# Kernel tuning notes

Hardware: AMD Instinct MI355X
Metric: run time of the kernel (lower is better)

Reference implementation:

```python
import jax, jax.numpy as jnp
import numpy as np

B, L, H, W, C = 2, 32, 16, 16, 32  # L must equal channels for the view() to be consistent
CH = L  # conv channel count


def setup_inputs() -> dict:
    key = jax.random.key(0)
    k1, k2, k3, k4, k5 = jax.random.split(key, 5)
    return {
        "inputs": jax.random.normal(k1, (B, L, H, W, C), dtype=jnp.float32),
        "W1": jax.random.normal(k2, (CH // 2, CH), dtype=jnp.float32) * 0.1,
        "b1": jax.random.normal(k3, (CH // 2,), dtype=jnp.float32) * 0.1,
        "W2": jax.random.normal(k4, (CH, CH), dtype=jnp.float32) * 0.1,
        "b2": jax.random.normal(k5, (CH,), dtype=jnp.float32) * 0.1,
        "gamma": jnp.ones((1,), dtype=jnp.float32),
    }


def reference(inputs, W1, b1, W2, b2, gamma):
    b, l, h, w, c = inputs.shape
    n = l * h * w  # flattened 'spatial' positions after the (buggy-but-faithful) reshape
    # conv1x1 over dim-1 (torch Conv3d treats dim-1 as channels)
    x1 = jnp.einsum('ol,blhwc->bohwc', W1, inputs) + b1[None, :, None, None, None]
    # permute (0,4,1,2,3) then view(b, c//2, l*h*w)
    x1 = jnp.transpose(x1, (0, 4, 1, 2, 3)).reshape(b, c // 2, n)
    # attn[b, i, j] = sum_k x1[b, k, i] * x1[b, k, j]; softmax over last dim
    attn = jax.nn.softmax(jnp.einsum('bki,bkj->bij', x1, x1), axis=-1)  # [b, n, n]
    x2 = jnp.einsum('ol,blhwc->bohwc', W2, inputs) + b2[None, :, None, None, None]
    x2 = jnp.transpose(x2, (0, 4, 1, 2, 3)).reshape(b, c, n)
    # x2 @ attn^T : out[b, c, i] = sum_j x2[b, c, j] * attn[b, i, j]
    out = jnp.einsum('bcj,bij->bci', x2, attn)
    out = jnp.transpose(out.reshape(b, c, l, h, w), (0, 2, 3, 4, 1))
    return out * gamma + inputs
```

## Files before the change

kernel.cpp:

```cpp
#include <hip/hip_runtime.h>
#include <hip/hip_bf16.h>
#include <math.h>

typedef __bf16 bf16x8 __attribute__((ext_vector_type(8)));
typedef __bf16 bf16x2 __attribute__((ext_vector_type(2)));
typedef short  s16x2  __attribute__((ext_vector_type(2)));
typedef short  s16x4  __attribute__((ext_vector_type(4)));
typedef float  floatx16 __attribute__((ext_vector_type(16)));

#define KQ_ELEMS (2 * 8192 * 16)
#define OACC_OFF 1572864
#define SQRT_LOG2E 1.2011224087864498f
#define LSPLIT 4

__global__ __launch_bounds__(256) void proj_kernel(
    const float* __restrict__ in, const float* __restrict__ W1,
    const float* __restrict__ b1, const float* __restrict__ W2,
    const float* __restrict__ b2,
    __hip_bfloat16* __restrict__ Kq, __hip_bfloat16* __restrict__ Vswz,
    float* __restrict__ acc0)
{
    __shared__ float Xs[32][32];
    __shared__ float W1s[16 * 32];
    __shared__ float W2s[32 * 32];
    const int t = threadIdx.x;
    const int bid = blockIdx.x;
    const int b = bid >> 8;
    const int hw = bid & 255;

    {
        int gid = bid * 256 + t;
        *(float4*)(acc0 + (size_t)gid * 4) = make_float4(0.f, 0.f, 0.f, 0.f);
        if (gid < 4096)
            *(float4*)(acc0 + 524288 + (size_t)gid * 4) = make_float4(0.f, 0.f, 0.f, 0.f);
    }

    {
        int l = t >> 3, cs = (t & 7) * 4;
        float4 v = *(const float4*)(in + (((size_t)b * 32 + l) * 256 + hw) * 32 + cs);
        *(float4*)&Xs[l][cs] = v;
    }
    if (t < 128) *(float4*)&W1s[t * 4] = *(const float4*)(W1 + t * 4);
    *(float4*)&W2s[t * 4] = *(const float4*)(W2 + t * 4);
    __syncthreads();

    const int c = t & 31;
    const int g = t >> 5;

#pragma unroll
    for (int oo = 0; oo < 2; ++oo) {
        int o = g * 2 + oo;
        float acc = b1[o];
#pragma unroll
        for (int l = 0; l < 32; ++l) acc += W1s[o * 32 + l] * Xs[l][c];
        int k = c >> 1;
        int i = (c & 1) * 4096 + o * 256 + hw;
        Kq[((size_t)b * 8192 + i) * 16 + k] = __float2bfloat16(acc * SQRT_LOG2E);
    }
#pragma unroll
    for (int oo = 0; oo < 4; ++oo) {
        int o = g * 4 + oo;
        float acc = b2[o];
#pragma unroll
        for (int l = 0; l < 32; ++l) acc += W2s[o * 32 + l] * Xs[l][c];
        int j = o * 256 + hw;
        int jt = j >> 5, rem = j & 31;
        int gg = rem >> 3, h = (rem >> 2) & 1, idx = rem & 3;
        Vswz[(size_t)b * 262144 + jt * 1024 + gg * 256 + h * 128 + c * 4 + idx] =
            __float2bfloat16(acc);
    }
}

__global__ __launch_bounds__(256) void flash_kernel(
    const __hip_bfloat16* __restrict__ Kq, const __hip_bfloat16* __restrict__ Vswz,
    float* __restrict__ Oacc, float* __restrict__ Lacc)
{
    const int t = threadIdx.x;
    const int lane = t & 63;
    const int wv = t >> 6;
    const int m = lane & 31;
    const int h = lane >> 5;

    const int bid = blockIdx.x;
    const int s = bid & ((1 << LSPLIT) - 1);
    const int itile = (bid >> LSPLIT) & 63;
    const int b = bid >> (LSPLIT + 6);
    const int i0 = itile * 128 + wv * 32;
    const int niter = (8192 >> LSPLIT) >> 5;
    const int jt0 = s * niter;

    const __hip_bfloat16* Kb = Kq + (size_t)b * 8192 * 16;
    const __hip_bfloat16* Vb = Vswz + (size_t)b * 262144 + h * 128 + m * 4;

    const bf16x8 bq = *(const bf16x8*)(Kb + (size_t)(i0 + m) * 16 + h * 8);

    floatx16 oa = {}, ob = {};
    float2 l01 = {0.f, 0.f}, l23 = {0.f, 0.f};

    bf16x8 ak = *(const bf16x8*)(Kb + (size_t)(jt0 * 32 + m) * 16 + h * 8);
    s16x4 vf0 = *(const s16x4*)(Vb + (size_t)jt0 * 1024 + 0);
    s16x4 vf1 = *(const s16x4*)(Vb + (size_t)jt0 * 1024 + 256);
    s16x4 vf2 = *(const s16x4*)(Vb + (size_t)jt0 * 1024 + 512);
    s16x4 vf3 = *(const s16x4*)(Vb + (size_t)jt0 * 1024 + 768);

    for (int it = 0; it < niter; ++it) {
        const int jtn = jt0 + (it + 1 < niter ? it + 1 : it);
        bf16x8 ak_n = *(const bf16x8*)(Kb + (size_t)(jtn * 32 + m) * 16 + h * 8);
        s16x4 vn0 = *(const s16x4*)(Vb + (size_t)jtn * 1024 + 0);
        s16x4 vn1 = *(const s16x4*)(Vb + (size_t)jtn * 1024 + 256);
        s16x4 vn2 = *(const s16x4*)(Vb + (size_t)jtn * 1024 + 512);
        s16x4 vn3 = *(const s16x4*)(Vb + (size_t)jtn * 1024 + 768);

        floatx16 sc = __builtin_amdgcn_mfma_f32_32x32x16_bf16(ak, bq, (floatx16){}, 0, 0, 0);

#pragma unroll
        for (int g = 0; g < 4; ++g) {
            float e0 = __builtin_amdgcn_exp2f(sc[4 * g + 0]);
            float e1 = __builtin_amdgcn_exp2f(sc[4 * g + 1]);
            float e2 = __builtin_amdgcn_exp2f(sc[4 * g + 2]);
            float e3 = __builtin_amdgcn_exp2f(sc[4 * g + 3]);
            l01.x += e0; l01.y += e1; l23.x += e2; l23.y += e3;
#if defined(__has_builtin) && __has_builtin(__builtin_amdgcn_cvt_pk_bf16_f32)
            bf16x2 plo = __builtin_amdgcn_cvt_pk_bf16_f32(e0, e1);
            bf16x2 phi = __builtin_amdgcn_cvt_pk_bf16_f32(e2, e3);
#else
            bf16x2 plo = {(__bf16)e0, (__bf16)e1};
            bf16x2 phi = {(__bf16)e2, (__bf16)e3};
#endif
            s16x2 lo = __builtin_bit_cast(s16x2, plo);
            s16x2 hi = __builtin_bit_cast(s16x2, phi);
            s16x4 pb = {lo[0], lo[1], hi[0], hi[1]};
            s16x4 vf = (g == 0) ? vf0 : (g == 1) ? vf1 : (g == 2) ? vf2 : vf3;
            if (g < 2)
                oa = __builtin_amdgcn_mfma_f32_32x32x8bf16_1k(pb, vf, oa, 0, 0, 0);
            else
                ob = __builtin_amdgcn_mfma_f32_32x32x8bf16_1k(pb, vf, ob, 0, 0, 0);
        }
        ak = ak_n; vf0 = vn0; vf1 = vn1; vf2 = vn2; vf3 = vn3;
    }

    oa = oa + ob;
    float l = (l01.x + l01.y) + (l23.x + l23.y);
    l += __shfl_xor(l, 32);

#pragma unroll
    for (int r = 0; r < 16; ++r) {
        int iloc = (r & 3) + 8 * (r >> 2) + 4 * h;
        size_t row = (size_t)b * 8192 + i0 + iloc;
        unsafeAtomicAdd(&Oacc[row * 32 + m], oa[r]);
    }
    if (h == 0)
        unsafeAtomicAdd(&Lacc[(size_t)b * 8192 + i0 + m], l);
}

__global__ __launch_bounds__(256) void finalize_kernel(
    const float* __restrict__ Oacc, const float* __restrict__ Lacc,
    const float* __restrict__ in, const float* __restrict__ gamma,
    float* __restrict__ out)
{
    const int t = threadIdx.x;
    const int c = t & 31;
    const size_t row = (size_t)blockIdx.x * 8 + (t >> 5);
    size_t idx = row * 32 + c;
    out[idx] = (Oacc[idx] / Lacc[row]) * gamma[0] + in[idx];
}

extern "C" void kernel_launch(void* const* d_in, const int* in_sizes, int n_in,
                              void* d_out, int out_size, void* d_ws, size_t ws_size,
                              hipStream_t stream) {
    const float* in = (const float*)d_in[0];
    const float* W1 = (const float*)d_in[1];
    const float* b1 = (const float*)d_in[2];
    const float* W2 = (const float*)d_in[3];
    const float* b2 = (const float*)d_in[4];
    const float* gamma = (const float*)d_in[5];
    float* out = (float*)d_out;

    __hip_bfloat16* Kq = (__hip_bfloat16*)d_ws;
    __hip_bfloat16* Vswz = Kq + KQ_ELEMS;
    float* Oacc = (float*)((char*)d_ws + OACC_OFF);
    float* Lacc = Oacc + 16384 * 32;

    proj_kernel<<<512, 256, 0, stream>>>(in, W1, b1, W2, b2, Kq, Vswz, Oacc);
    flash_kernel<<<2 * 64 * (1 << LSPLIT), 256, 0, stream>>>(Kq, Vswz, Oacc, Lacc);
    finalize_kernel<<<2048, 256, 0, stream>>>(Oacc, Lacc, in, gamma, out);
}
```

Measured before the change: 112.4 us.

## Fuse finalize into flash kernel via last-block atomic counter

Measured after the change: 270.2 us. +140.5%, slower.

```diff
diff --git a/kernel.cpp b/kernel.cpp
--- a/kernel.cpp
+++ b/kernel.cpp
@@ -31,7 +31,7 @@
     {
         int gid = bid * 256 + t;
         *(float4*)(acc0 + (size_t)gid * 4) = make_float4(0.f, 0.f, 0.f, 0.f);
-        if (gid < 4096)
+        if (gid < 4160)
             *(float4*)(acc0 + 524288 + (size_t)gid * 4) = make_float4(0.f, 0.f, 0.f, 0.f);
     }
 
@@ -73,7 +73,9 @@
 
 __global__ __launch_bounds__(256) void flash_kernel(
     const __hip_bfloat16* __restrict__ Kq, const __hip_bfloat16* __restrict__ Vswz,
-    float* __restrict__ Oacc, float* __restrict__ Lacc)
+    float* __restrict__ Oacc, float* __restrict__ Lacc, int* __restrict__ Cnt,
+    const float* __restrict__ in, const float* __restrict__ gamma,
+    float* __restrict__ out)
 {
     const int t = threadIdx.x;
     const int lane = t & 63;
@@ -151,18 +153,24 @@
     }
     if (h == 0)
         unsafeAtomicAdd(&Lacc[(size_t)b * 8192 + i0 + m], l);
-}
 
-__global__ __launch_bounds__(256) void finalize_kernel(
-    const float* __restrict__ Oacc, const float* __restrict__ Lacc,
-    const float* __restrict__ in, const float* __restrict__ gamma,
-    float* __restrict__ out)
-{
-    const int t = threadIdx.x;
-    const int c = t & 31;
-    const size_t row = (size_t)blockIdx.x * 8 + (t >> 5);
-    size_t idx = row * 32 + c;
-    out[idx] = (Oacc[idx] / Lacc[row]) * gamma[0] + in[idx];
+    __threadfence();
+    __syncthreads();
+    __shared__ int sflag;
+    if (t == 0) sflag = atomicAdd(&Cnt[b * 64 + itile], 1);
+    __syncthreads();
+    if (sflag == (1 << LSPLIT) - 1) {
+        const float gm = gamma[0];
+        const size_t rbase = (size_t)b * 8192 + itile * 128;
+        const size_t fbase = rbase * 32;
+        for (int e = t; e < 4096; e += 256) {
+            float ov = __hip_atomic_load(&Oacc[fbase + e], __ATOMIC_RELAXED,
+                                         __HIP_MEMORY_SCOPE_AGENT);
+            float lv = __hip_atomic_load(&Lacc[rbase + (e >> 5)], __ATOMIC_RELAXED,
+                                         __HIP_MEMORY_SCOPE_AGENT);
+            out[fbase + e] = (ov / lv) * gm + in[fbase + e];
+        }
+    }
 }
 
 extern "C" void kernel_launch(void* const* d_in, const int* in_sizes, int n_in,
@@ -180,8 +188,9 @@
     __hip_bfloat16* Vswz = Kq + KQ_ELEMS;
     float* Oacc = (float*)((char*)d_ws + OACC_OFF);
     float* Lacc = Oacc + 16384 * 32;
+    int* Cnt = (int*)(Lacc + 16384);
 
     proj_kernel<<<512, 256, 0, stream>>>(in, W1, b1, W2, b2, Kq, Vswz, Oacc);
-    flash_kernel<<<2 * 64 * (1 << LSPLIT), 256, 0, stream>>>(Kq, Vswz, Oacc, Lacc);
-    finalize_kernel<<<2048, 256, 0, stream>>>(Oacc, Lacc, in, gamma, out);
+    flash_kernel<<<2 * 64 * (1 << LSPLIT), 256, 0, stream>>>(Kq, Vswz, Oacc, Lacc, Cnt,
+                                                             in, gamma, out);
 }
```

## Switch flash attention to 16x16x16 MFMA tiles with new V swizzle layout

Applied to the files above, without the earlier changes.

After: 127.1 us. 1.13x slower.

```diff
diff --git a/kernel.cpp b/kernel.cpp
--- a/kernel.cpp
+++ b/kernel.cpp
@@ -2,16 +2,15 @@
 #include <hip/hip_bf16.h>
 #include <math.h>
 
-typedef __bf16 bf16x8 __attribute__((ext_vector_type(8)));
 typedef __bf16 bf16x2 __attribute__((ext_vector_type(2)));
 typedef short  s16x2  __attribute__((ext_vector_type(2)));
 typedef short  s16x4  __attribute__((ext_vector_type(4)));
-typedef float  floatx16 __attribute__((ext_vector_type(16)));
+typedef float  floatx4 __attribute__((ext_vector_type(4)));
 
 #define KQ_ELEMS (2 * 8192 * 16)
 #define OACC_OFF 1572864
 #define SQRT_LOG2E 1.2011224087864498f
-#define LSPLIT 4
+#define LSPLIT 3
 
 __global__ __launch_bounds__(256) void proj_kernel(
     const float* __restrict__ in, const float* __restrict__ W1,
@@ -64,9 +63,8 @@
 #pragma unroll
         for (int l = 0; l < 32; ++l) acc += W2s[o * 32 + l] * Xs[l][c];
         int j = o * 256 + hw;
-        int jt = j >> 5, rem = j & 31;
-        int gg = rem >> 3, h = (rem >> 2) & 1, idx = rem & 3;
-        Vswz[(size_t)b * 262144 + jt * 1024 + gg * 256 + h * 128 + c * 4 + idx] =
+        int jt = j >> 4, q = (j >> 2) & 3, idx = j & 3;
+        Vswz[(size_t)b * 262144 + jt * 512 + (c >> 4) * 256 + q * 64 + (c & 15) * 4 + idx] =
             __float2bfloat16(acc);
     }
 }
@@ -78,78 +76,70 @@
     const int t = threadIdx.x;
     const int lane = t & 63;
     const int wv = t >> 6;
-    const int m = lane & 31;
-    const int h = lane >> 5;
+    const int m = lane & 15;
+    const int q = lane >> 4;
 
     const int bid = blockIdx.x;
     const int s = bid & ((1 << LSPLIT) - 1);
-    const int itile = (bid >> LSPLIT) & 63;
-    const int b = bid >> (LSPLIT + 6);
-    const int i0 = itile * 128 + wv * 32;
-    const int niter = (8192 >> LSPLIT) >> 5;
+    const int itile = (bid >> LSPLIT) & 127;
+    const int b = bid >> (LSPLIT + 7);
+    const int i0 = itile * 64 + wv * 16;
+    const int niter = (8192 >> LSPLIT) >> 4;
     const int jt0 = s * niter;
 
     const __hip_bfloat16* Kb = Kq + (size_t)b * 8192 * 16;
-    const __hip_bfloat16* Vb = Vswz + (size_t)b * 262144 + h * 128 + m * 4;
+    const __hip_bfloat16* Vb = Vswz + (size_t)b * 262144 + lane * 4;
 
-    const bf16x8 bq = *(const bf16x8*)(Kb + (size_t)(i0 + m) * 16 + h * 8);
+    const s16x4 bq = *(const s16x4*)(Kb + (size_t)(i0 + m) * 16 + q * 4);
 
-    floatx16 oa = {}, ob = {};
-    float2 l01 = {0.f, 0.f}, l23 = {0.f, 0.f};
+    floatx4 oa = {}, ob = {};
+    float2 l01 = {0.f, 0.f};
 
-    bf16x8 ak = *(const bf16x8*)(Kb + (size_t)(jt0 * 32 + m) * 16 + h * 8);
-    s16x4 vf0 = *(const s16x4*)(Vb + (size_t)jt0 * 1024 + 0);
-    s16x4 vf1 = *(const s16x4*)(Vb + (size_t)jt0 * 1024 + 256);
-    s16x4 vf2 = *(const s16x4*)(Vb + (size_t)jt0 * 1024 + 512);
-    s16x4 vf3 = *(const s16x4*)(Vb + (size_t)jt0 * 1024 + 768);
+    s16x4 ak = *(const s16x4*)(Kb + (size_t)(jt0 * 16 + m) * 16 + q * 4);
+    s16x4 v0 = *(const s16x4*)(Vb + (size_t)jt0 * 512 + 0);
+    s16x4 v1 = *(const s16x4*)(Vb + (size_t)jt0 * 512 + 256);
 
     for (int it = 0; it < niter; ++it) {
         const int jtn = jt0 + (it + 1 < niter ? it + 1 : it);
-        bf16x8 ak_n = *(const bf16x8*)(Kb + (size_t)(jtn * 32 + m) * 16 + h * 8);
-        s16x4 vn0 = *(const s16x4*)(Vb + (size_t)jtn * 1024 + 0);
-        s16x4 vn1 = *(const s16x4*)(Vb + (size_t)jtn * 1024 + 256);
-        s16x4 vn2 = *(const s16x4*)(Vb + (size_t)jtn * 1024 + 512);
-        s16x4 vn3 = *(const s16x4*)(Vb + (size_t)jtn * 1024 + 768);
+        s16x4 ak_n = *(const s16x4*)(Kb + (size_t)(jtn * 16 + m) * 16 + q * 4);
+        s16x4 vn0 = *(const s16x4*)(Vb + (size_t)jtn * 512 + 0);
+        s16x4 vn1 = *(const s16x4*)(Vb + (size_t)jtn * 512 + 256);
 
-        floatx16 sc = __builtin_amdgcn_mfma_f32_32x32x16_bf16(ak, bq, (floatx16){}, 0, 0, 0);
+        floatx4 sc = __builtin_amdgcn_mfma_f32_16x16x16bf16_1k(ak, bq, (floatx4){}, 0, 0, 0);
 
-#pragma unroll
-        for (int g = 0; g < 4; ++g) {
-            float e0 = __builtin_amdgcn_exp2f(sc[4 * g + 0]);
-            float e1 = __builtin_amdgcn_exp2f(sc[4 * g + 1]);
-            float e2 = __builtin_amdgcn_exp2f(sc[4 * g + 2]);
-            float e3 = __builtin_amdgcn_exp2f(sc[4 * g + 3]);
-            l01.x += e0; l01.y += e1; l23.x += e2; l23.y += e3;
+        float e0 = __builtin_amdgcn_exp2f(sc[0]);
+        float e1 = __builtin_amdgcn_exp2f(sc[1]);
+        float e2 = __builtin_amdgcn_exp2f(sc[2]);
+        float e3 = __builtin_amdgcn_exp2f(sc[3]);
+        l01.x += e0 + e2; l01.y += e1 + e3;
 #if defined(__has_builtin) && __has_builtin(__builtin_amdgcn_cvt_pk_bf16_f32)
-            bf16x2 plo = __builtin_amdgcn_cvt_pk_bf16_f32(e0, e1);
-            bf16x2 phi = __builtin_amdgcn_cvt_pk_bf16_f32(e2, e3);
+        bf16x2 plo = __builtin_amdgcn_cvt_pk_bf16_f32(e0, e1);
+        bf16x2 phi = __builtin_amdgcn_cvt_pk_bf16_f32(e2, e3);
 #else
-            bf16x2 plo = {(__bf16)e0, (__bf16)e1};
-            bf16x2 phi = {(__bf16)e2, (__bf16)e3};
+        bf16x2 plo = {(__bf16)e0, (__bf16)e1};
+        bf16x2 phi = {(__bf16)e2, (__bf16)e3};
 #endif
-            s16x2 lo = __builtin_bit_cast(s16x2, plo);
-            s16x2 hi = __builtin_bit_cast(s16x2, phi);
-            s16x4 pb = {lo[0], lo[1], hi[0], hi[1]};
-            s16x4 vf = (g == 0) ? vf0 : (g == 1) ? vf1 : (g == 2) ? vf2 : vf3;
-            if (g < 2)
-                oa = __builtin_amdgcn_mfma_f32_32x32x8bf16_1k(pb, vf, oa, 0, 0, 0);
-            else
-                ob = __builtin_amdgcn_mfma_f32_32x32x8bf16_1k(pb, vf, ob, 0, 0, 0);
-        }
-        ak = ak_n; vf0 = vn0; vf1 = vn1; vf2 = vn2; vf3 = vn3;
+        s16x2 lo = __builtin_bit_cast(s16x2, plo);
+        s16x2 hi = __builtin_bit_cast(s16x2, phi);
+        s16x4 pb = {lo[0], lo[1], hi[0], hi[1]};
+
+        oa = __builtin_amdgcn_mfma_f32_16x16x16bf16_1k(pb, v0, oa, 0, 0, 0);
+        ob = __builtin_amdgcn_mfma_f32_16x16x16bf16_1k(pb, v1, ob, 0, 0, 0);
+
+        ak = ak_n; v0 = vn0; v1 = vn1;
     }
 
-    oa = oa + ob;
-    float l = (l01.x + l01.y) + (l23.x + l23.y);
+    float l = l01.x + l01.y;
+    l += __shfl_xor(l, 16);
     l += __shfl_xor(l, 32);
 
 #pragma unroll
-    for (int r = 0; r < 16; ++r) {
-        int iloc = (r & 3) + 8 * (r >> 2) + 4 * h;
-        size_t row = (size_t)b * 8192 + i0 + iloc;
+    for (int r = 0; r < 4; ++r) {
+        size_t row = (size_t)b * 8192 + i0 + 4 * q + r;
         unsafeAtomicAdd(&Oacc[row * 32 + m], oa[r]);
+        unsafeAtomicAdd(&Oacc[row * 32 + 16 + m], ob[r]);
     }
-    if (h == 0)
+    if (lane < 16)
         unsafeAtomicAdd(&Lacc[(size_t)b * 8192 + i0 + m], l);
 }
 
@@ -182,6 +172,6 @@
     float* Lacc = Oacc + 16384 * 32;
 
     proj_kernel<<<512, 256, 0, stream>>>(in, W1, b1, W2, b2, Kq, Vswz, Oacc);
-    flash_kernel<<<2 * 64 * (1 << LSPLIT), 256, 0, stream>>>(Kq, Vswz, Oacc, Lacc);
+    flash_kernel<<<2 * 128 * (1 << LSPLIT), 256, 0, stream>>>(Kq, Vswz, Oacc, Lacc);
     finalize_kernel<<<2048, 256, 0, stream>>>(Oacc, Lacc, in, gamma, out);
 }
```
